# Performance work log

Hardware: AMD Instinct MI355X
Metric: run time of the kernel (lower is better)

The kernel has to match this reference:

```python
import jax, jax.numpy as jnp
import numpy as np

B, C, L, H = 2, 512, 4096, 8
D = C // H  # depth per head


def setup_inputs() -> dict:
    key = jax.random.key(0)
    k1, k2, k3 = jax.random.split(key, 3)
    queries = jax.random.normal(k1, (B, C, L), dtype=jnp.float32)
    mask = jnp.ones((B, L), dtype=jnp.int32)
    # xavier-ish scaling for stability
    Wm = jax.random.normal(k2, (2 * C, C), dtype=jnp.float32) * (1.0 / np.sqrt(C))
    Wq = jax.random.normal(k3, (C, C), dtype=jnp.float32) * (1.0 / np.sqrt(C))
    return {"queries": queries, "mask": mask, "Wm": Wm, "Wq": Wq}


def reference(queries, mask, Wm, Wq):
    # 1x1 conv projections == channel matmuls on [B, C, L]
    q = jnp.einsum('oc,bcl->bol', Wq, queries)   # [B, C, L]
    m = jnp.einsum('oc,bcl->bol', Wm, queries)   # [B, 2C, L]
    # to [B, L, *], split heads -> [B, H, L, D]
    qh = q.transpose(0, 2, 1).reshape(B, L, H, D).transpose(0, 2, 1, 3)
    mem = m.transpose(0, 2, 1)                   # [B, L, 2C]
    k, v = jnp.split(mem, 2, axis=2)             # each [B, L, C]
    kh = k.reshape(B, L, H, D).transpose(0, 2, 1, 3)
    vh = v.reshape(B, L, H, D).transpose(0, 2, 1, 3)
    qh = qh * (D ** -0.5)
    logits = jnp.einsum('bhqd,bhkd->bhqk', qh, kh)          # [B, H, L, L]
    mf = mask.astype(jnp.float32)[:, None, None, :]          # [B, 1, 1, L]
    logits = logits + (-1e30) * (1.0 - mf)
    weights = jax.nn.softmax(logits, axis=-1)                # dropout is identity in eval
    out = jnp.einsum('bhqk,bhkd->bhqd', weights, vh)         # [B, H, L, D]
    # combine heads -> [B, L, C] -> [B, C, L]
    return out.transpose(0, 2, 1, 3).reshape(B, L, C).transpose(0, 2, 1)
```

## Files before the change

### kernel.cpp

```cpp
#include <hip/hip_runtime.h>

#define Bn 2
#define Cn 512
#define Ln 4096
#define Hn 8
#define Dn 64

typedef _Float16 f16;
typedef _Float16 h8 __attribute__((ext_vector_type(8)));
typedef _Float16 h4 __attribute__((ext_vector_type(4)));
typedef float f32x4 __attribute__((ext_vector_type(4)));

#define MFMA32(a, b, c) __builtin_amdgcn_mfma_f32_16x16x32_f16(a, b, c, 0, 0, 0)
#define MFMA16(a, b, c) __builtin_amdgcn_mfma_f32_16x16x16f16(a, b, c, 0, 0, 0)
#define AS1(p) ((const __attribute__((address_space(1))) void*)(p))
#define AS3(p) ((__attribute__((address_space(3))) void*)(p))

__global__ __launch_bounds__(256) void k_transpose(const float* __restrict__ X,
                                                   f16* __restrict__ Xt) {
  int bid = blockIdx.x;
  int b  = bid >> 9;
  int r  = bid & 511;
  int lt = r >> 3, ct = r & 7;
  int l0 = lt << 6, c0 = ct << 6;
  __shared__ f16 t[64][66];
  int tid = threadIdx.x;
  int lx = tid & 63, cg = tid >> 6;
  const float* xb = X + ((size_t)b * Cn) * Ln;
#pragma unroll
  for (int rr = 0; rr < 16; ++rr) {
    int cl = cg * 16 + rr;
    t[lx][cl] = (f16)xb[(size_t)(c0 + cl) * Ln + l0 + lx];
  }
  __syncthreads();
  f16* xo = Xt + ((size_t)b * Ln + l0) * Cn + c0;
  int cx = tid & 63, lg = tid >> 6;
#pragma unroll
  for (int rr = 0; rr < 16; ++rr) {
    int ll = lg * 16 + rr;
    xo[(size_t)ll * Cn + cx] = t[ll][cx];
  }
}

__global__ __launch_bounds__(256) void k_proj(const float* __restrict__ Wq,
                                              const float* __restrict__ Wm,
                                              const f16* __restrict__ Xt,
                                              f16* __restrict__ Qd,
                                              f16* __restrict__ Kd,
                                              f16* __restrict__ Vv) {
  int bid = blockIdx.x;
  int b = bid / 384;
  int r = bid % 384;
  int mt = r >> 5, nt = r & 31;
  int o0 = mt << 7, l0 = nt << 7;
  __shared__ f16 a_lds[128][40];
  __shared__ f16 b_lds[128][40];
  int tid = threadIdx.x;
  int lane = tid & 63, w = tid >> 6;
  int wr = w >> 1, wc = w & 1;
  f32x4 acc[4][4] = {};

  int sr = tid >> 1;
  int scg = (tid & 1) << 4;
  int o_s = o0 + sr;
  const float* wrow = (o_s < 512) ? (Wq + (size_t)o_s * Cn)
                                  : (Wm + (size_t)(o_s - 512) * Cn);
  const f16* xrow = Xt + ((size_t)b * Ln + l0 + sr) * Cn;

  for (int kt = 0; kt < 16; ++kt) {
    int c0 = kt << 5;
    __syncthreads();
#pragma unroll
    for (int i = 0; i < 4; ++i) {
      float4 w4 = *(const float4*)(wrow + c0 + scg + 4 * i);
      h4 hh = { (f16)w4.x, (f16)w4.y, (f16)w4.z, (f16)w4.w };
      *(h4*)&a_lds[sr][scg + 4 * i] = hh;
    }
#pragma unroll
    for (int i = 0; i < 2; ++i)
      *(h8*)&b_lds[sr][scg + 8 * i] = *(const h8*)(xrow + c0 + scg + 8 * i);
    __syncthreads();

    h8 af[4], bf[4];
#pragma unroll
    for (int mi = 0; mi < 4; ++mi)
      af[mi] = *(const h8*)&a_lds[wr * 64 + mi * 16 + (lane & 15)][(lane >> 4) * 8];
#pragma unroll
    for (int ni = 0; ni < 4; ++ni)
      bf[ni] = *(const h8*)&b_lds[wc * 64 + ni * 16 + (lane & 15)][(lane >> 4) * 8];
#pragma unroll
    for (int mi = 0; mi < 4; ++mi)
#pragma unroll
      for (int ni = 0; ni < 4; ++ni)
        acc[mi][ni] = MFMA32(af[mi], bf[ni], acc[mi][ni]);
  }

  const float QSCALE = 0.18033688011112042f;
  int lrow = (lane >> 4) << 2;
  int lcol = lane & 15;
#pragma unroll
  for (int mi = 0; mi < 4; ++mi) {
    int ob = o0 + wr * 64 + mi * 16 + lrow;
#pragma unroll
    for (int ni = 0; ni < 4; ++ni) {
      int lc = l0 + wc * 64 + ni * 16 + lcol;
      f32x4 a = acc[mi][ni];
      if (ob < 512) {
        int h = ob >> 6, d = ob & 63;
        h4 hh = { (f16)(a[0] * QSCALE), (f16)(a[1] * QSCALE),
                  (f16)(a[2] * QSCALE), (f16)(a[3] * QSCALE) };
        *(h4*)&Qd[(((size_t)b * Hn + h) * Ln + lc) * Dn + d] = hh;
      } else if (ob < 1024) {
        int oc = ob - 512;
        int h = oc >> 6, d = oc & 63;
        h4 hh = { (f16)a[0], (f16)a[1], (f16)a[2], (f16)a[3] };
        *(h4*)&Kd[(((size_t)b * Hn + h) * Ln + lc) * Dn + d] = hh;
      } else {
        int oc = ob - 1024;
#pragma unroll
        for (int rr = 0; rr < 4; ++rr)
          Vv[((size_t)b * Cn + oc + rr) * Ln + lc] = (f16)a[rr];
      }
    }
  }
}

__global__ __launch_bounds__(256, 4) void k_attn(const f16* __restrict__ Qd,
                                                 const f16* __restrict__ Kd,
                                                 const f16* __restrict__ Vv,
                                                 const int* __restrict__ mask,
                                                 float* __restrict__ out) {
  int bid0 = blockIdx.x;
  int bid = (bid0 & 7) * 128 + (bid0 >> 3);
  int bh = bid >> 6, ib = bid & 63;
  int b = bh >> 3, h = bh & 7;
  int tid = threadIdx.x;
  int lane = tid & 63, w = tid >> 6;
  int il = lane & 15, g = lane >> 4;

  __shared__ __align__(16) f16 kbuf[2][64 * 64];
  __shared__ __align__(16) f16 vbuf[2][64 * 64];

  const h8* qsrc = (const h8*)(Qd + ((size_t)bh * Ln + ib * 64 + w * 16 + il) * Dn);
  h8 bq0 = qsrc[g];
  h8 bq1 = qsrc[4 + g];

  const int* mbase = mask + (size_t)b * Ln;
  unsigned long long flags;
  {
    const int4* mp = (const int4*)mbase + lane * 16;
    int ac = 1;
#pragma unroll
    for (int q = 0; q < 16; ++q) { int4 v = mp[q]; ac &= v.x & v.y & v.z & v.w; }
    flags = __ballot(ac == 1);
  }

  const f16* kbase = Kd + (size_t)bh * Ln * Dn;
  const f16* vbase = Vv + ((size_t)b * Cn + h * 64) * Ln;
  int koff[2], voff[2];
#pragma unroll
  for (int q = 0; q < 2; ++q) {
    int rr = w * 16 + q * 8 + (lane >> 3);
    int swz = (lane & 7) ^ (rr & 7);
    koff[q] = rr * 64 + swz * 8;
    voff[q] = rr * Ln + swz * 8;
  }

#define STAGE(bufi, t)                                                          \
  {                                                                             \
    _Pragma("unroll")                                                           \
    for (int q = 0; q < 2; ++q) {                                               \
      __builtin_amdgcn_global_load_lds(AS1(kbase + (size_t)(t) * 4096 + koff[q]),\
                                       AS3(&kbuf[bufi][(w * 16 + q * 8) * 64]), \
                                       16, 0, 0);                               \
      __builtin_amdgcn_global_load_lds(AS1(vbase + (size_t)(t) * 64 + voff[q]), \
                                       AS3(&vbuf[bufi][(w * 16 + q * 8) * 64]), \
                                       16, 0, 0);                               \
    }                                                                           \
  }

  f32x4 acc[4] = {};
  float mrow = -1e38f;
  float lsum = 0.f;

  STAGE(0, 0);
  asm volatile("s_waitcnt vmcnt(0)" ::: "memory");
  __builtin_amdgcn_s_barrier();

  int cur = 0;
  for (int t = 0; t < 64; ++t) {
    if (t < 63) STAGE(cur ^ 1, t + 1);

    const f16* kl = kbuf[cur];
    f32x4 s[4];
#pragma unroll
    for (int T = 0; T < 4; ++T) {
      int row = (T * 16 + il) * 64;
      h8 a0 = *(const h8*)&kl[row + ((g ^ (lane & 7)) << 3)];
      h8 a1 = *(const h8*)&kl[row + (((4 + g) ^ (lane & 7)) << 3)];
      f32x4 z = {};
      z = MFMA32(a0, bq0, z);
      z = MFMA32(a1, bq1, z);
      s[T] = z;
    }

    if (!((flags >> t) & 1)) {
#pragma unroll
      for (int T = 0; T < 4; ++T) {
        int4 mk = *(const int4*)(mbase + t * 64 + T * 16 + g * 4);
        s[T][0] = mk.x ? s[T][0] : -3.0e4f;
        s[T][1] = mk.y ? s[T][1] : -3.0e4f;
        s[T][2] = mk.z ? s[T][2] : -3.0e4f;
        s[T][3] = mk.w ? s[T][3] : -3.0e4f;
      }
    }

    float mx;
    {
      float a = fmaxf(fmaxf(s[0][0], s[0][1]), fmaxf(s[0][2], s[0][3]));
      float b2 = fmaxf(fmaxf(s[1][0], s[1][1]), fmaxf(s[1][2], s[1][3]));
      float c = fmaxf(fmaxf(s[2][0], s[2][1]), fmaxf(s[2][2], s[2][3]));
      float d = fmaxf(fmaxf(s[3][0], s[3][1]), fmaxf(s[3][2], s[3][3]));
      mx = fmaxf(fmaxf(a, b2), fmaxf(c, d));
    }
    mx = fmaxf(mx, __shfl_xor(mx, 16));
    mx = fmaxf(mx, __shfl_xor(mx, 32));

    if (__any(mx > mrow + 8.f)) {
      float mn = fmaxf(mrow, mx);
      float al = __builtin_amdgcn_exp2f(mrow - mn);
      lsum *= al;
#pragma unroll
      for (int tt = 0; tt < 4; ++tt) {
        f32x4 a = acc[tt];
        a[0] *= al; a[1] *= al; a[2] *= al; a[3] *= al;
        acc[tt] = a;
      }
      mrow = mn;
    }

    h4 pa[4];
    float rs = 0.f;
#pragma unroll
    for (int T = 0; T < 4; ++T) {
      float p0 = __builtin_amdgcn_exp2f(s[T][0] - mrow);
      float p1 = __builtin_amdgcn_exp2f(s[T][1] - mrow);
      float p2 = __builtin_amdgcn_exp2f(s[T][2] - mrow);
      float p3 = __builtin_amdgcn_exp2f(s[T][3] - mrow);
      h4 hh = { (f16)p0, (f16)p1, (f16)p2, (f16)p3 };
      pa[T] = hh;
      rs += (p0 + p1) + (p2 + p3);
    }
    rs += __shfl_xor(rs, 16);
    rs += __shfl_xor(rs, 32);
    lsum += rs;

    const f16* vl = vbuf[cur];
#pragma unroll
    for (int tt = 0; tt < 4; ++tt) {
      int drow = tt * 16 + il;
#pragma unroll
      for (int T = 0; T < 4; ++T) {
        int chunk = T * 2 + (g >> 1);
        h4 va = *(const h4*)&vl[drow * 64 + ((chunk ^ (drow & 7)) << 3) + ((g & 1) << 2)];
        acc[tt] = MFMA16(va, pa[T], acc[tt]);
      }
    }

    asm volatile("s_waitcnt vmcnt(0)" ::: "memory");
    __builtin_amdgcn_s_barrier();
    cur ^= 1;
  }

  float inv = 1.f / lsum;
  size_t obase = ((size_t)b * Cn + h * 64) * Ln + ib * 64 + w * 16 + il;
#pragma unroll
  for (int tt = 0; tt < 4; ++tt)
#pragma unroll
    for (int rr = 0; rr < 4; ++rr) {
      int d = tt * 16 + g * 4 + rr;
      out[obase + (size_t)d * Ln] = acc[tt][rr] * inv;
    }
}

extern "C" void kernel_launch(void* const* d_in, const int* in_sizes, int n_in,
                              void* d_out, int out_size, void* d_ws, size_t ws_size,
                              hipStream_t stream) {
  const float* queries = (const float*)d_in[0];
  const int*   mask    = (const int*)d_in[1];
  const float* Wm      = (const float*)d_in[2];
  const float* Wq      = (const float*)d_in[3];
  float* out = (float*)d_out;
  char* ws = (char*)d_ws;
  f16* Xt = (f16*)(ws);
  f16* Qd = (f16*)(ws + 8388608);
  f16* Kd = (f16*)(ws + 16777216);
  f16* Vv = (f16*)(ws + 25165824);

  k_transpose<<<1024, 256, 0, stream>>>(queries, Xt);
  k_proj<<<768, 256, 0, stream>>>(Wq, Wm, Xt, Qd, Kd, Vv);
  k_attn<<<16 * 64, 256, 0, stream>>>(Qd, Kd, Vv, mask, out);
}
```

Before: 163.9 us.

## Process two query tiles per wave to reuse K/V loads in attention

Each wave now handles 32 query rows (two 16-row tiles) instead of 16, so every block covers 128 queries and the grid shrinks from 1024 to 512 blocks. Each K/V tile staged in LDS and each LDS fragment read is reused by twice as many MFMAs, which halves global K/V traffic and LDS reads per query. The cost is higher register pressure, so launch bounds drop to 2 blocks per CU. Fewer blocks also means less parallelism and a longer per-block dependency chain. A swizzle index changes from lane&7 to il&7; these are equal because il is lane&15.

```diff
diff --git a/kernel.cpp b/kernel.cpp
--- a/kernel.cpp
+++ b/kernel.cpp
@@ -125,14 +125,14 @@
   }
 }
 
-__global__ __launch_bounds__(256, 4) void k_attn(const f16* __restrict__ Qd,
+__global__ __launch_bounds__(256, 2) void k_attn(const f16* __restrict__ Qd,
                                                  const f16* __restrict__ Kd,
                                                  const f16* __restrict__ Vv,
                                                  const int* __restrict__ mask,
                                                  float* __restrict__ out) {
   int bid0 = blockIdx.x;
-  int bid = (bid0 & 7) * 128 + (bid0 >> 3);
-  int bh = bid >> 6, ib = bid & 63;
+  int bid = (bid0 & 7) * 64 + (bid0 >> 3);
+  int bh = bid >> 5, ib = bid & 31;
   int b = bh >> 3, h = bh & 7;
   int tid = threadIdx.x;
   int lane = tid & 63, w = tid >> 6;
@@ -141,9 +141,11 @@
   __shared__ __align__(16) f16 kbuf[2][64 * 64];
   __shared__ __align__(16) f16 vbuf[2][64 * 64];
 
-  const h8* qsrc = (const h8*)(Qd + ((size_t)bh * Ln + ib * 64 + w * 16 + il) * Dn);
-  h8 bq0 = qsrc[g];
-  h8 bq1 = qsrc[4 + g];
+  int qb = ib * 128 + w * 32;
+  const h8* qsA = (const h8*)(Qd + ((size_t)bh * Ln + qb + il) * Dn);
+  const h8* qsB = (const h8*)(Qd + ((size_t)bh * Ln + qb + 16 + il) * Dn);
+  h8 bqA0 = qsA[g], bqA1 = qsA[4 + g];
+  h8 bqB0 = qsB[g], bqB1 = qsB[4 + g];
 
   const int* mbase = mask + (size_t)b * Ln;
   unsigned long long flags;
@@ -179,9 +181,9 @@
     }                                                                           \
   }
 
-  f32x4 acc[4] = {};
-  float mrow = -1e38f;
-  float lsum = 0.f;
+  f32x4 accA[4] = {}, accB[4] = {};
+  float mA = -1e38f, mB = -1e38f;
+  float lA = 0.f, lB = 0.f;
 
   STAGE(0, 0);
   asm volatile("s_waitcnt vmcnt(0)" ::: "memory");
@@ -192,68 +194,106 @@
     if (t < 63) STAGE(cur ^ 1, t + 1);
 
     const f16* kl = kbuf[cur];
-    f32x4 s[4];
+    f32x4 sA[4], sB[4];
 #pragma unroll
     for (int T = 0; T < 4; ++T) {
       int row = (T * 16 + il) * 64;
-      h8 a0 = *(const h8*)&kl[row + ((g ^ (lane & 7)) << 3)];
-      h8 a1 = *(const h8*)&kl[row + (((4 + g) ^ (lane & 7)) << 3)];
-      f32x4 z = {};
-      z = MFMA32(a0, bq0, z);
-      z = MFMA32(a1, bq1, z);
-      s[T] = z;
+      h8 a0 = *(const h8*)&kl[row + ((g ^ (il & 7)) << 3)];
+      h8 a1 = *(const h8*)&kl[row + (((4 + g) ^ (il & 7)) << 3)];
+      f32x4 zA = {}, zB = {};
+      zA = MFMA32(a0, bqA0, zA);
+      zA = MFMA32(a1, bqA1, zA);
+      zB = MFMA32(a0, bqB0, zB);
+      zB = MFMA32(a1, bqB1, zB);
+      sA[T] = zA; sB[T] = zB;
     }
 
     if (!((flags >> t) & 1)) {
 #pragma unroll
       for (int T = 0; T < 4; ++T) {
         int4 mk = *(const int4*)(mbase + t * 64 + T * 16 + g * 4);
-        s[T][0] = mk.x ? s[T][0] : -3.0e4f;
-        s[T][1] = mk.y ? s[T][1] : -3.0e4f;
-        s[T][2] = mk.z ? s[T][2] : -3.0e4f;
-        s[T][3] = mk.w ? s[T][3] : -3.0e4f;
-      }
-    }
-
-    float mx;
+        sA[T][0] = mk.x ? sA[T][0] : -3.0e4f;
+        sA[T][1] = mk.y ? sA[T][1] : -3.0e4f;
+        sA[T][2] = mk.z ? sA[T][2] : -3.0e4f;
+        sA[T][3] = mk.w ? sA[T][3] : -3.0e4f;
+        sB[T][0] = mk.x ? sB[T][0] : -3.0e4f;
+        sB[T][1] = mk.y ? sB[T][1] : -3.0e4f;
+        sB[T][2] = mk.z ? sB[T][2] : -3.0e4f;
+        sB[T][3] = mk.w ? sB[T][3] : -3.0e4f;
+      }
+    }
+
+    h4 paA[4], paB[4];
     {
-      float a = fmaxf(fmaxf(s[0][0], s[0][1]), fmaxf(s[0][2], s[0][3]));
-      float b2 = fmaxf(fmaxf(s[1][0], s[1][1]), fmaxf(s[1][2], s[1][3]));
-      float c = fmaxf(fmaxf(s[2][0], s[2][1]), fmaxf(s[2][2], s[2][3]));
-      float d = fmaxf(fmaxf(s[3][0], s[3][1]), fmaxf(s[3][2], s[3][3]));
-      mx = fmaxf(fmaxf(a, b2), fmaxf(c, d));
-    }
-    mx = fmaxf(mx, __shfl_xor(mx, 16));
-    mx = fmaxf(mx, __shfl_xor(mx, 32));
-
-    if (__any(mx > mrow + 8.f)) {
-      float mn = fmaxf(mrow, mx);
-      float al = __builtin_amdgcn_exp2f(mrow - mn);
-      lsum *= al;
-#pragma unroll
-      for (int tt = 0; tt < 4; ++tt) {
-        f32x4 a = acc[tt];
-        a[0] *= al; a[1] *= al; a[2] *= al; a[3] *= al;
-        acc[tt] = a;
-      }
-      mrow = mn;
-    }
-
-    h4 pa[4];
-    float rs = 0.f;
-#pragma unroll
-    for (int T = 0; T < 4; ++T) {
-      float p0 = __builtin_amdgcn_exp2f(s[T][0] - mrow);
-      float p1 = __builtin_amdgcn_exp2f(s[T][1] - mrow);
-      float p2 = __builtin_amdgcn_exp2f(s[T][2] - mrow);
-      float p3 = __builtin_amdgcn_exp2f(s[T][3] - mrow);
-      h4 hh = { (f16)p0, (f16)p1, (f16)p2, (f16)p3 };
-      pa[T] = hh;
-      rs += (p0 + p1) + (p2 + p3);
-    }
-    rs += __shfl_xor(rs, 16);
-    rs += __shfl_xor(rs, 32);
-    lsum += rs;
+      float a = fmaxf(fmaxf(sA[0][0], sA[0][1]), fmaxf(sA[0][2], sA[0][3]));
+      float b2 = fmaxf(fmaxf(sA[1][0], sA[1][1]), fmaxf(sA[1][2], sA[1][3]));
+      float c = fmaxf(fmaxf(sA[2][0], sA[2][1]), fmaxf(sA[2][2], sA[2][3]));
+      float d = fmaxf(fmaxf(sA[3][0], sA[3][1]), fmaxf(sA[3][2], sA[3][3]));
+      float mx = fmaxf(fmaxf(a, b2), fmaxf(c, d));
+      mx = fmaxf(mx, __shfl_xor(mx, 16));
+      mx = fmaxf(mx, __shfl_xor(mx, 32));
+      if (__any(mx > mA + 8.f)) {
+        float mn = fmaxf(mA, mx);
+        float al = __builtin_amdgcn_exp2f(mA - mn);
+        lA *= al;
+#pragma unroll
+        for (int tt = 0; tt < 4; ++tt) {
+          f32x4 a4 = accA[tt];
+          a4[0] *= al; a4[1] *= al; a4[2] *= al; a4[3] *= al;
+          accA[tt] = a4;
+        }
+        mA = mn;
+      }
+      float rs = 0.f;
+#pragma unroll
+      for (int T = 0; T < 4; ++T) {
+        float p0 = __builtin_amdgcn_exp2f(sA[T][0] - mA);
+        float p1 = __builtin_amdgcn_exp2f(sA[T][1] - mA);
+        float p2 = __builtin_amdgcn_exp2f(sA[T][2] - mA);
+        float p3 = __builtin_amdgcn_exp2f(sA[T][3] - mA);
+        h4 hh = { (f16)p0, (f16)p1, (f16)p2, (f16)p3 };
+        paA[T] = hh;
+        rs += (p0 + p1) + (p2 + p3);
+      }
+      rs += __shfl_xor(rs, 16);
+      rs += __shfl_xor(rs, 32);
+      lA += rs;
+    }
+    {
+      float a = fmaxf(fmaxf(sB[0][0], sB[0][1]), fmaxf(sB[0][2], sB[0][3]));
+      float b2 = fmaxf(fmaxf(sB[1][0], sB[1][1]), fmaxf(sB[1][2], sB[1][3]));
+      float c = fmaxf(fmaxf(sB[2][0], sB[2][1]), fmaxf(sB[2][2], sB[2][3]));
+      float d = fmaxf(fmaxf(sB[3][0], sB[3][1]), fmaxf(sB[3][2], sB[3][3]));
+      float mx = fmaxf(fmaxf(a, b2), fmaxf(c, d));
+      mx = fmaxf(mx, __shfl_xor(mx, 16));
+      mx = fmaxf(mx, __shfl_xor(mx, 32));
+      if (__any(mx > mB + 8.f)) {
+        float mn = fmaxf(mB, mx);
+        float al = __builtin_amdgcn_exp2f(mB - mn);
+        lB *= al;
+#pragma unroll
+        for (int tt = 0; tt < 4; ++tt) {
+          f32x4 a4 = accB[tt];
+          a4[0] *= al; a4[1] *= al; a4[2] *= al; a4[3] *= al;
+          accB[tt] = a4;
+        }
+        mB = mn;
+      }
+      float rs = 0.f;
+#pragma unroll
+      for (int T = 0; T < 4; ++T) {
+        float p0 = __builtin_amdgcn_exp2f(sB[T][0] - mB);
+        float p1 = __builtin_amdgcn_exp2f(sB[T][1] - mB);
+        float p2 = __builtin_amdgcn_exp2f(sB[T][2] - mB);
+        float p3 = __builtin_amdgcn_exp2f(sB[T][3] - mB);
+        h4 hh = { (f16)p0, (f16)p1, (f16)p2, (f16)p3 };
+        paB[T] = hh;
+        rs += (p0 + p1) + (p2 + p3);
+      }
+      rs += __shfl_xor(rs, 16);
+      rs += __shfl_xor(rs, 32);
+      lB += rs;
+    }
 
     const f16* vl = vbuf[cur];
 #pragma unroll
@@ -263,7 +303,8 @@
       for (int T = 0; T < 4; ++T) {
         int chunk = T * 2 + (g >> 1);
         h4 va = *(const h4*)&vl[drow * 64 + ((chunk ^ (drow & 7)) << 3) + ((g & 1) << 2)];
-        acc[tt] = MFMA16(va, pa[T], acc[tt]);
+        accA[tt] = MFMA16(va, paA[T], accA[tt]);
+        accB[tt] = MFMA16(va, paB[T], accB[tt]);
       }
     }
 
@@ -272,14 +313,16 @@
     cur ^= 1;
   }
 
-  float inv = 1.f / lsum;
-  size_t obase = ((size_t)b * Cn + h * 64) * Ln + ib * 64 + w * 16 + il;
+  float invA = 1.f / lA, invB = 1.f / lB;
+  size_t obA = ((size_t)b * Cn + h * 64) * Ln + qb + il;
+  size_t obB = obA + 16;
 #pragma unroll
   for (int tt = 0; tt < 4; ++tt)
 #pragma unroll
     for (int rr = 0; rr < 4; ++rr) {
       int d = tt * 16 + g * 4 + rr;
-      out[obase + (size_t)d * Ln] = acc[tt][rr] * inv;
+      out[obA + (size_t)d * Ln] = accA[tt][rr] * invA;
+      out[obB + (size_t)d * Ln] = accB[tt][rr] * invB;
     }
 }
 
@@ -299,5 +342,5 @@
 
   k_transpose<<<1024, 256, 0, stream>>>(queries, Xt);
   k_proj<<<768, 256, 0, stream>>>(Wq, Wm, Xt, Qd, Kd, Vv);
-  k_attn<<<16 * 64, 256, 0, stream>>>(Qd, Kd, Vv, mask, out);
+  k_attn<<<512, 256, 0, stream>>>(Qd, Kd, Vv, mask, out);
 }
```

New measurement: 158.4 us. 1.03x faster.

## Switch attention to 32x32x16 MFMA with 128-query blocks per workgroup

Applied to the files above, without the earlier changes.

The attention kernel now gives each wave 32 query rows and uses 32x32x16 f16 MFMAs for both QK^T and PV, so one K/V tile staged in LDS is reused across twice as many queries. The grid halves to 512 blocks, and the P fragments are rearranged between lane halves with cross-lane shuffles instead of being fed directly. s_setprio is raised around the MFMA sections. The aim is fewer LDS reads and less K/V traffic per FLOP, at the cost of more registers (occupancy hint lowered from 4 to 2) and fewer blocks to fill the GPU.

```diff
diff --git a/kernel.cpp b/kernel.cpp
--- a/kernel.cpp
+++ b/kernel.cpp
@@ -9,10 +9,12 @@
 typedef _Float16 f16;
 typedef _Float16 h8 __attribute__((ext_vector_type(8)));
 typedef _Float16 h4 __attribute__((ext_vector_type(4)));
+typedef _Float16 h2 __attribute__((ext_vector_type(2)));
 typedef float f32x4 __attribute__((ext_vector_type(4)));
+typedef float f32x16 __attribute__((ext_vector_type(16)));
 
 #define MFMA32(a, b, c) __builtin_amdgcn_mfma_f32_16x16x32_f16(a, b, c, 0, 0, 0)
-#define MFMA16(a, b, c) __builtin_amdgcn_mfma_f32_16x16x16f16(a, b, c, 0, 0, 0)
+#define MFMA3216(a, b, c) __builtin_amdgcn_mfma_f32_32x32x16_f16(a, b, c, 0, 0, 0)
 #define AS1(p) ((const __attribute__((address_space(1))) void*)(p))
 #define AS3(p) ((__attribute__((address_space(3))) void*)(p))
 
@@ -125,25 +127,28 @@
   }
 }
 
-__global__ __launch_bounds__(256, 4) void k_attn(const f16* __restrict__ Qd,
+__global__ __launch_bounds__(256, 2) void k_attn(const f16* __restrict__ Qd,
                                                  const f16* __restrict__ Kd,
                                                  const f16* __restrict__ Vv,
                                                  const int* __restrict__ mask,
                                                  float* __restrict__ out) {
   int bid0 = blockIdx.x;
-  int bid = (bid0 & 7) * 128 + (bid0 >> 3);
-  int bh = bid >> 6, ib = bid & 63;
+  int bid = (bid0 & 7) * 64 + (bid0 >> 3);
+  int bh = bid >> 5, ib = bid & 31;
   int b = bh >> 3, h = bh & 7;
   int tid = threadIdx.x;
   int lane = tid & 63, w = tid >> 6;
-  int il = lane & 15, g = lane >> 4;
+  int il = lane & 31, hi = lane >> 5;
 
   __shared__ __align__(16) f16 kbuf[2][64 * 64];
   __shared__ __align__(16) f16 vbuf[2][64 * 64];
 
-  const h8* qsrc = (const h8*)(Qd + ((size_t)bh * Ln + ib * 64 + w * 16 + il) * Dn);
-  h8 bq0 = qsrc[g];
-  h8 bq1 = qsrc[4 + g];
+  int qb = ib * 128 + w * 32;
+  const f16* qp = Qd + ((size_t)bh * Ln + qb + il) * Dn;
+  h8 qreg[4];
+#pragma unroll
+  for (int dt = 0; dt < 4; ++dt)
+    qreg[dt] = *(const h8*)(qp + dt * 16 + hi * 8);
 
   const int* mbase = mask + (size_t)b * Ln;
   unsigned long long flags;
@@ -179,7 +184,7 @@
     }                                                                           \
   }
 
-  f32x4 acc[4] = {};
+  f32x16 acc[2] = {};
   float mrow = -1e38f;
   float lsum = 0.f;
 
@@ -187,43 +192,49 @@
   asm volatile("s_waitcnt vmcnt(0)" ::: "memory");
   __builtin_amdgcn_s_barrier();
 
+  int swz7 = il & 7;
   int cur = 0;
   for (int t = 0; t < 64; ++t) {
     if (t < 63) STAGE(cur ^ 1, t + 1);
 
     const f16* kl = kbuf[cur];
-    f32x4 s[4];
-#pragma unroll
-    for (int T = 0; T < 4; ++T) {
-      int row = (T * 16 + il) * 64;
-      h8 a0 = *(const h8*)&kl[row + ((g ^ (lane & 7)) << 3)];
-      h8 a1 = *(const h8*)&kl[row + (((4 + g) ^ (lane & 7)) << 3)];
-      f32x4 z = {};
-      z = MFMA32(a0, bq0, z);
-      z = MFMA32(a1, bq1, z);
-      s[T] = z;
-    }
+    f32x16 s0 = {}, s1 = {};
+    __builtin_amdgcn_s_setprio(1);
+#pragma unroll
+    for (int dt = 0; dt < 4; ++dt) {
+      int c = ((dt * 2 + hi) ^ swz7) << 3;
+      h8 ak0 = *(const h8*)&kl[il * 64 + c];
+      h8 ak1 = *(const h8*)&kl[(32 + il) * 64 + c];
+      s0 = MFMA3216(ak0, qreg[dt], s0);
+      s1 = MFMA3216(ak1, qreg[dt], s1);
+    }
+    __builtin_amdgcn_s_setprio(0);
 
     if (!((flags >> t) & 1)) {
 #pragma unroll
-      for (int T = 0; T < 4; ++T) {
-        int4 mk = *(const int4*)(mbase + t * 64 + T * 16 + g * 4);
-        s[T][0] = mk.x ? s[T][0] : -3.0e4f;
-        s[T][1] = mk.y ? s[T][1] : -3.0e4f;
-        s[T][2] = mk.z ? s[T][2] : -3.0e4f;
-        s[T][3] = mk.w ? s[T][3] : -3.0e4f;
+      for (int r = 0; r < 16; ++r) {
+        int j = t * 64 + (r & 3) + 8 * (r >> 2) + 4 * hi;
+        if (!mbase[j])      s0[r] = -3.0e4f;
+        if (!mbase[j + 32]) s1[r] = -3.0e4f;
       }
     }
 
     float mx;
     {
-      float a = fmaxf(fmaxf(s[0][0], s[0][1]), fmaxf(s[0][2], s[0][3]));
-      float b2 = fmaxf(fmaxf(s[1][0], s[1][1]), fmaxf(s[1][2], s[1][3]));
-      float c = fmaxf(fmaxf(s[2][0], s[2][1]), fmaxf(s[2][2], s[2][3]));
-      float d = fmaxf(fmaxf(s[3][0], s[3][1]), fmaxf(s[3][2], s[3][3]));
+      float m0 = fmaxf(s0[0], s0[1]), m1 = fmaxf(s0[2], s0[3]);
+      float m2 = fmaxf(s0[4], s0[5]), m3 = fmaxf(s0[6], s0[7]);
+      float m4 = fmaxf(s0[8], s0[9]), m5 = fmaxf(s0[10], s0[11]);
+      float m6 = fmaxf(s0[12], s0[13]), m7 = fmaxf(s0[14], s0[15]);
+      float n0 = fmaxf(s1[0], s1[1]), n1 = fmaxf(s1[2], s1[3]);
+      float n2 = fmaxf(s1[4], s1[5]), n3 = fmaxf(s1[6], s1[7]);
+      float n4 = fmaxf(s1[8], s1[9]), n5 = fmaxf(s1[10], s1[11]);
+      float n6 = fmaxf(s1[12], s1[13]), n7 = fmaxf(s1[14], s1[15]);
+      float a = fmaxf(fmaxf(m0, m1), fmaxf(m2, m3));
+      float b2 = fmaxf(fmaxf(m4, m5), fmaxf(m6, m7));
+      float c = fmaxf(fmaxf(n0, n1), fmaxf(n2, n3));
+      float d = fmaxf(fmaxf(n4, n5), fmaxf(n6, n7));
       mx = fmaxf(fmaxf(a, b2), fmaxf(c, d));
     }
-    mx = fmaxf(mx, __shfl_xor(mx, 16));
     mx = fmaxf(mx, __shfl_xor(mx, 32));
 
     if (__any(mx > mrow + 8.f)) {
@@ -231,41 +242,61 @@
       float al = __builtin_amdgcn_exp2f(mrow - mn);
       lsum *= al;
 #pragma unroll
-      for (int tt = 0; tt < 4; ++tt) {
-        f32x4 a = acc[tt];
-        a[0] *= al; a[1] *= al; a[2] *= al; a[3] *= al;
-        acc[tt] = a;
-      }
+      for (int r = 0; r < 16; ++r) { acc[0][r] *= al; acc[1][r] *= al; }
       mrow = mn;
     }
 
-    h4 pa[4];
+#pragma unroll
+    for (int r = 0; r < 16; ++r) {
+      s0[r] = __builtin_amdgcn_exp2f(s0[r] - mrow);
+      s1[r] = __builtin_amdgcn_exp2f(s1[r] - mrow);
+    }
+
     float rs = 0.f;
 #pragma unroll
-    for (int T = 0; T < 4; ++T) {
-      float p0 = __builtin_amdgcn_exp2f(s[T][0] - mrow);
-      float p1 = __builtin_amdgcn_exp2f(s[T][1] - mrow);
-      float p2 = __builtin_amdgcn_exp2f(s[T][2] - mrow);
-      float p3 = __builtin_amdgcn_exp2f(s[T][3] - mrow);
-      h4 hh = { (f16)p0, (f16)p1, (f16)p2, (f16)p3 };
-      pa[T] = hh;
-      rs += (p0 + p1) + (p2 + p3);
-    }
-    rs += __shfl_xor(rs, 16);
+    for (int r = 0; r < 16; r += 4) {
+      rs += ((s0[r] + s0[r + 1]) + (s0[r + 2] + s0[r + 3]));
+      rs += ((s1[r] + s1[r + 1]) + (s1[r + 2] + s1[r + 3]));
+    }
     rs += __shfl_xor(rs, 32);
     lsum += rs;
 
+    float dw0[8], dw1[8];
+#pragma unroll
+    for (int r = 0; r < 16; r += 2) {
+      dw0[r >> 1] = __builtin_bit_cast(float, __builtin_amdgcn_cvt_pkrtz(s0[r], s0[r + 1]));
+      dw1[r >> 1] = __builtin_bit_cast(float, __builtin_amdgcn_cvt_pkrtz(s1[r], s1[r + 1]));
+    }
+
+    h8 pb[4];
+#pragma unroll
+    for (int jt = 0; jt < 4; ++jt) {
+      const float* dd = (jt < 2) ? dw0 : dw1;
+      int base = (jt & 1) * 4;
+      float x0 = dd[base + 0], x1 = dd[base + 1];
+      float y0 = dd[base + 2], y1 = dd[base + 3];
+      float v0 = hi ? x0 : y0, v1 = hi ? x1 : y1;
+      float p0 = __shfl_xor(v0, 32), p1 = __shfl_xor(v1, 32);
+      union { h8 v; float f[4]; } u;
+      u.f[0] = hi ? p0 : x0;
+      u.f[1] = hi ? p1 : x1;
+      u.f[2] = hi ? y0 : p0;
+      u.f[3] = hi ? y1 : p1;
+      pb[jt] = u.v;
+    }
+
     const f16* vl = vbuf[cur];
-#pragma unroll
-    for (int tt = 0; tt < 4; ++tt) {
-      int drow = tt * 16 + il;
-#pragma unroll
-      for (int T = 0; T < 4; ++T) {
-        int chunk = T * 2 + (g >> 1);
-        h4 va = *(const h4*)&vl[drow * 64 + ((chunk ^ (drow & 7)) << 3) + ((g & 1) << 2)];
-        acc[tt] = MFMA16(va, pa[T], acc[tt]);
+    __builtin_amdgcn_s_setprio(1);
+#pragma unroll
+    for (int dt = 0; dt < 2; ++dt) {
+      int rv = dt * 32 + il;
+#pragma unroll
+      for (int jt = 0; jt < 4; ++jt) {
+        h8 av = *(const h8*)&vl[rv * 64 + (((jt * 2 + hi) ^ swz7) << 3)];
+        acc[dt] = MFMA3216(av, pb[jt], acc[dt]);
       }
     }
+    __builtin_amdgcn_s_setprio(0);
 
     asm volatile("s_waitcnt vmcnt(0)" ::: "memory");
     __builtin_amdgcn_s_barrier();
@@ -273,13 +304,13 @@
   }
 
   float inv = 1.f / lsum;
-  size_t obase = ((size_t)b * Cn + h * 64) * Ln + ib * 64 + w * 16 + il;
-#pragma unroll
-  for (int tt = 0; tt < 4; ++tt)
-#pragma unroll
-    for (int rr = 0; rr < 4; ++rr) {
-      int d = tt * 16 + g * 4 + rr;
-      out[obase + (size_t)d * Ln] = acc[tt][rr] * inv;
+  size_t obase = ((size_t)b * Cn + h * 64) * Ln + qb + il;
+#pragma unroll
+  for (int dt = 0; dt < 2; ++dt)
+#pragma unroll
+    for (int r = 0; r < 16; ++r) {
+      int d = dt * 32 + (r & 3) + 8 * (r >> 2) + 4 * hi;
+      out[obase + (size_t)d * Ln] = acc[dt][r] * inv;
     }
 }
 
@@ -299,5 +330,5 @@
 
   k_transpose<<<1024, 256, 0, stream>>>(queries, Xt);
   k_proj<<<768, 256, 0, stream>>>(Wq, Wm, Xt, Qd, Kd, Vv);
-  k_attn<<<16 * 64, 256, 0, stream>>>(Qd, Kd, Vv, mask, out);
+  k_attn<<<512, 256, 0, stream>>>(Qd, Kd, Vv, mask, out);
 }
```

After: 145.9 us. 11.0% less time.
